# Optimization experiments

Hardware: AMD Instinct MI355X
Metric: run time of the kernel (lower is better)

The kernel has to match this reference:

```python
import jax, jax.numpy as jnp
import numpy as np

N_NODES = 50000
N_EDGES = 1600000
IN_DIM = 1024
MID_DIM = 256


def setup_inputs() -> dict:
    key = jax.random.key(0)
    k1, k2, k3, k4 = jax.random.split(key, 4)
    x = jax.random.normal(k1, (N_NODES, IN_DIM), dtype=jnp.float32)
    edge_index = jax.random.randint(k2, (2, N_EDGES), 0, N_NODES, dtype=jnp.int64)
    # Glorot-style init like PyG GCNConv
    W1 = jax.random.normal(k3, (IN_DIM, MID_DIM), dtype=jnp.float32) * (2.0 / (IN_DIM + MID_DIM)) ** 0.5
    W2 = jax.random.normal(k4, (MID_DIM, IN_DIM), dtype=jnp.float32) * (2.0 / (MID_DIM + IN_DIM)) ** 0.5
    b1 = jnp.zeros((MID_DIM,), dtype=jnp.float32)
    b2 = jnp.zeros((IN_DIM,), dtype=jnp.float32)
    return {"x": x, "edge_index": edge_index, "W1": W1, "b1": b1, "W2": W2, "b2": b2}


def _gcn_conv(x, W, b, src, dst, norm, n):
    # PyG GCNConv: linear transform first, then normalized neighbor sum, then bias.
    xw = x @ W                                   # [N, F_out]
    msg = xw[src] * norm[:, None]                # gather + scale, [E+N, F_out]
    out = jax.ops.segment_sum(msg, dst, num_segments=n)
    return out + b


def reference(x, edge_index, W1, b1, W2, b2):
    n = x.shape[0]
    loops = jnp.arange(n, dtype=edge_index.dtype)
    src = jnp.concatenate([edge_index[0], loops])
    dst = jnp.concatenate([edge_index[1], loops])
    # symmetric normalization with self-loops: D^-1/2 (A+I) D^-1/2
    deg = jax.ops.segment_sum(jnp.ones_like(dst, dtype=x.dtype), dst, num_segments=n)
    dis = jnp.where(deg > 0, jax.lax.rsqrt(jnp.maximum(deg, 1.0)), 0.0)
    norm = dis[src] * dis[dst]                   # [E+N]
    h = jax.nn.relu(_gcn_conv(x, W1, b1, src, dst, norm, n))
    # F.dropout(training=False) is identity at inference
    out = _gcn_conv(h, W2, b2, src, dst, norm, n)
    return out
```

## Files before the change

### kernel.cpp

```cpp
#include <hip/hip_runtime.h>

typedef unsigned short u16;
typedef u16 u16x8 __attribute__((ext_vector_type(8)));
typedef u16 u16x4 __attribute__((ext_vector_type(4)));
typedef short s16x8 __attribute__((ext_vector_type(8)));
typedef float f32x4 __attribute__((ext_vector_type(4)));

__device__ __forceinline__ float b2f(u16 u) {
  unsigned int v = ((unsigned int)u) << 16;
  return __builtin_bit_cast(float, v);
}
__device__ __forceinline__ u16 f2b(float f) {
  unsigned int u = __builtin_bit_cast(unsigned int, f);
  u += 0x7FFFu + ((u >> 16) & 1u);
  return (u16)(u >> 16);
}

__global__ void deg_kernel(const int* __restrict__ dst, int* __restrict__ deg, int E, int n) {
  int e = blockIdx.x * 256 + threadIdx.x;
  if (e < E) {
    int d = dst[e];
    d = min(max(d, 0), n - 1);
    atomicAdd(&deg[d], 1);
  }
}

__global__ void dis_kernel(const int* __restrict__ deg, float* __restrict__ dis, int n) {
  int i = blockIdx.x * 256 + threadIdx.x;
  if (i < n) dis[i] = 1.0f / sqrtf((float)(deg[i] + 1));
}

__global__ __launch_bounds__(256) void scanA(const int* __restrict__ cnt, int* __restrict__ bsum, int n) {
  __shared__ int s[256];
  int t = threadIdx.x, i = blockIdx.x * 256 + t;
  s[t] = (i < n) ? cnt[i] : 0;
  __syncthreads();
  for (int off = 128; off > 0; off >>= 1) {
    if (t < off) s[t] += s[t + off];
    __syncthreads();
  }
  if (t == 0) bsum[blockIdx.x] = s[0];
}

__global__ __launch_bounds__(256) void scanB(int* __restrict__ bsum, int nb) {
  __shared__ int s[256];
  int t = threadIdx.x;
  int v = (t < nb) ? bsum[t] : 0;
  s[t] = v;
  __syncthreads();
  for (int off = 1; off < 256; off <<= 1) {
    int x = (t >= off) ? s[t - off] : 0;
    __syncthreads();
    s[t] += x;
    __syncthreads();
  }
  if (t < nb) bsum[t] = s[t] - v;
}

__global__ __launch_bounds__(256) void scanC(const int* __restrict__ cnt, const int* __restrict__ bsum,
                                             int* __restrict__ rowp, int n) {
  __shared__ int s[256];
  int t = threadIdx.x, i = blockIdx.x * 256 + t;
  int v = (i < n) ? cnt[i] : 0;
  s[t] = v;
  __syncthreads();
  for (int off = 1; off < 256; off <<= 1) {
    int x = (t >= off) ? s[t - off] : 0;
    __syncthreads();
    s[t] += x;
    __syncthreads();
  }
  if (i < n) rowp[i + 1] = bsum[blockIdx.x] + s[t];
  if (i == 0) rowp[0] = 0;
}

__global__ void fill_kernel(const int* __restrict__ src, const int* __restrict__ dst,
                            const int* __restrict__ rowp, int* __restrict__ fill,
                            const float* __restrict__ dis, int* __restrict__ csr_s,
                            float* __restrict__ csr_w, int E, int n) {
  int e = blockIdx.x * 256 + threadIdx.x;
  if (e < E) {
    int s = src[e]; s = min(max(s, 0), n - 1);
    int d = dst[e]; d = min(max(d, 0), n - 1);
    int pos = rowp[d] + atomicAdd(&fill[d], 1);
    csr_s[pos] = s;
    csr_w[pos] = dis[s] * dis[d];
  }
}

__global__ void transpose_cvt(const float* __restrict__ in, u16* __restrict__ out, int K, int N) {
  int idx = blockIdx.x * 256 + threadIdx.x;
  if (idx < K * N) {
    int k = idx / N, nn = idx - k * N;
    out[(size_t)nn * K + k] = f2b(in[idx]);
  }
}

template <bool A_F32, bool OUT_F32>
__global__ __launch_bounds__(256) void gemm_kernel(const void* __restrict__ Ap,
                                                   const u16* __restrict__ BT,
                                                   const float* __restrict__ bias,
                                                   void* __restrict__ Cp, int M, int N, int K) {
  __shared__ u16 As[2][128 * 40];
  __shared__ u16 Bs[2][128 * 40];
  const int tid = threadIdx.x;
  const int m0 = blockIdx.y * 128, n0 = blockIdx.x * 128;
  const int lane = tid & 63, wv = tid >> 6;
  const int wr = (wv >> 1) * 64, wc = (wv & 1) * 64;
  const int q = lane >> 4, l = lane & 15;
  f32x4 acc[4][4] = {};

  float4 aregf[4];
  u16x8 aregb[2];
  u16x8 breg[2];

  auto load_tile = [&](int kt) {
    if (A_F32) {
      const float* A = (const float*)Ap;
#pragma unroll
      for (int i = 0; i < 4; i++) {
        int t = tid + i * 256;
        int r = t >> 3, k4 = (t & 7) * 4;
        int gr = m0 + r;
        aregf[i] = make_float4(0.f, 0.f, 0.f, 0.f);
        if (gr < M) aregf[i] = *(const float4*)&A[(size_t)gr * K + kt + k4];
      }
    } else {
      const u16* A = (const u16*)Ap;
#pragma unroll
      for (int i = 0; i < 2; i++) {
        int t = tid + i * 256;
        int r = t >> 2, k8 = (t & 3) * 8;
        int gr = m0 + r;
        aregb[i] = (u16x8){};
        if (gr < M) aregb[i] = *(const u16x8*)&A[(size_t)gr * K + kt + k8];
      }
    }
#pragma unroll
    for (int i = 0; i < 2; i++) {
      int t = tid + i * 256;
      int r = t >> 2, k8 = (t & 3) * 8;
      breg[i] = *(const u16x8*)&BT[(size_t)(n0 + r) * K + kt + k8];
    }
  };

  auto store_tile = [&](int buf) {
    if (A_F32) {
#pragma unroll
      for (int i = 0; i < 4; i++) {
        int t = tid + i * 256;
        int r = t >> 3, k4 = (t & 7) * 4;
        u16x4 o;
        o[0] = f2b(aregf[i].x); o[1] = f2b(aregf[i].y);
        o[2] = f2b(aregf[i].z); o[3] = f2b(aregf[i].w);
        *(u16x4*)&As[buf][r * 40 + k4] = o;
      }
    } else {
#pragma unroll
      for (int i = 0; i < 2; i++) {
        int t = tid + i * 256;
        int r = t >> 2, k8 = (t & 3) * 8;
        *(u16x8*)&As[buf][r * 40 + k8] = aregb[i];
      }
    }
#pragma unroll
    for (int i = 0; i < 2; i++) {
      int t = tid + i * 256;
      int r = t >> 2, k8 = (t & 3) * 8;
      *(u16x8*)&Bs[buf][r * 40 + k8] = breg[i];
    }
  };

  load_tile(0);
  store_tile(0);
  __syncthreads();

  int cur = 0;
  for (int kt = 0; kt < K; kt += 32) {
    const bool has_next = (kt + 32) < K;
    if (has_next) load_tile(kt + 32);

    s16x8 af[4], bf[4];
#pragma unroll
    for (int mi = 0; mi < 4; mi++) af[mi] = *(const s16x8*)&As[cur][(wr + mi * 16 + l) * 40 + q * 8];
#pragma unroll
    for (int ni = 0; ni < 4; ni++) bf[ni] = *(const s16x8*)&Bs[cur][(wc + ni * 16 + l) * 40 + q * 8];
#pragma unroll
    for (int mi = 0; mi < 4; mi++)
#pragma unroll
      for (int ni = 0; ni < 4; ni++)
        acc[mi][ni] = __builtin_amdgcn_mfma_f32_16x16x32_bf16(af[mi], bf[ni], acc[mi][ni], 0, 0, 0);

    if (has_next) store_tile(cur ^ 1);
    __syncthreads();
    cur ^= 1;
  }

#pragma unroll
  for (int ni = 0; ni < 4; ni++) {
    int col = n0 + wc + ni * 16 + l;
    float bv = bias ? bias[col] : 0.f;
#pragma unroll
    for (int mi = 0; mi < 4; mi++) {
#pragma unroll
      for (int j = 0; j < 4; j++) {
        int row = m0 + wr + mi * 16 + q * 4 + j;
        if (row < M) {
          float v = acc[mi][ni][j] + bv;
          if (OUT_F32)
            ((float*)Cp)[(size_t)row * N + col] = v;
          else
            ((u16*)Cp)[(size_t)row * N + col] = f2b(v);
        }
      }
    }
  }
}

template <bool RELU>
__global__ __launch_bounds__(256) void agg_kernel(const u16* __restrict__ tab,
                                                  const int* __restrict__ rowp,
                                                  const int* __restrict__ csr_s,
                                                  const float* __restrict__ csr_w,
                                                  const float* __restrict__ dis,
                                                  const float* __restrict__ bias,
                                                  u16* __restrict__ out, int n) {
  int wv = threadIdx.x >> 6, lane = threadIdx.x & 63;
  int node = blockIdx.x * 4 + wv;
  if (node >= n) return;
  int f0 = lane * 4;
  float sw = dis[node];
  sw *= sw;
  u16x4 v = *(const u16x4*)&tab[(size_t)node * 256 + f0];
  float a0 = sw * b2f(v[0]), a1 = sw * b2f(v[1]), a2 = sw * b2f(v[2]), a3 = sw * b2f(v[3]);
  int e0 = rowp[node], e1 = rowp[node + 1];
  int e = e0;
  for (; e + 4 <= e1; e += 4) {
    int s0 = csr_s[e], s1 = csr_s[e + 1], s2 = csr_s[e + 2], s3 = csr_s[e + 3];
    float w0 = csr_w[e], w1 = csr_w[e + 1], w2 = csr_w[e + 2], w3 = csr_w[e + 3];
    u16x4 u0 = *(const u16x4*)&tab[(size_t)s0 * 256 + f0];
    u16x4 u1 = *(const u16x4*)&tab[(size_t)s1 * 256 + f0];
    u16x4 u2 = *(const u16x4*)&tab[(size_t)s2 * 256 + f0];
    u16x4 u3 = *(const u16x4*)&tab[(size_t)s3 * 256 + f0];
    a0 += w0 * b2f(u0[0]) + w1 * b2f(u1[0]) + w2 * b2f(u2[0]) + w3 * b2f(u3[0]);
    a1 += w0 * b2f(u0[1]) + w1 * b2f(u1[1]) + w2 * b2f(u2[1]) + w3 * b2f(u3[1]);
    a2 += w0 * b2f(u0[2]) + w1 * b2f(u1[2]) + w2 * b2f(u2[2]) + w3 * b2f(u3[2]);
    a3 += w0 * b2f(u0[3]) + w1 * b2f(u1[3]) + w2 * b2f(u2[3]) + w3 * b2f(u3[3]);
  }
  for (; e < e1; e++) {
    int s = csr_s[e];
    float w = csr_w[e];
    u16x4 u = *(const u16x4*)&tab[(size_t)s * 256 + f0];
    a0 += w * b2f(u[0]);
    a1 += w * b2f(u[1]);
    a2 += w * b2f(u[2]);
    a3 += w * b2f(u[3]);
  }
  if (RELU) {
    a0 = fmaxf(a0 + bias[f0 + 0], 0.f);
    a1 = fmaxf(a1 + bias[f0 + 1], 0.f);
    a2 = fmaxf(a2 + bias[f0 + 2], 0.f);
    a3 = fmaxf(a3 + bias[f0 + 3], 0.f);
  }
  u16x4 o;
  o[0] = f2b(a0); o[1] = f2b(a1); o[2] = f2b(a2); o[3] = f2b(a3);
  *(u16x4*)&out[(size_t)node * 256 + f0] = o;
}

extern "C" void kernel_launch(void* const* d_in, const int* in_sizes, int n_in,
                              void* d_out, int out_size, void* d_ws, size_t ws_size,
                              hipStream_t stream) {
  const float* x  = (const float*)d_in[0];
  const int*   ei = (const int*)d_in[1];
  const float* W1 = (const float*)d_in[2];
  const float* b1 = (const float*)d_in[3];
  const float* W2 = (const float*)d_in[4];
  const float* b2 = (const float*)d_in[5];

  const int MID = in_sizes[3];
  const int IN  = in_sizes[5];
  const int n   = in_sizes[0] / IN;
  const int E   = in_sizes[1] / 2;
  const int* srcv = ei;
  const int* dstv = ei + E;

  char* w = (char*)d_ws;
  size_t off = 0;
  auto alloc = [&](size_t bytes) -> void* {
    void* p = w + off;
    off += (bytes + 255) & ~(size_t)255;
    return p;
  };
  int*   deg   = (int*)alloc((size_t)n * 4);
  int*   rowp  = (int*)alloc((size_t)(n + 1) * 4);
  int*   fill  = (int*)alloc((size_t)n * 4);
  int*   bsum  = (int*)alloc(1024);
  int*   csr_s = (int*)alloc((size_t)E * 4);
  float* csr_w = (float*)alloc((size_t)E * 4);
  float* dis   = (float*)alloc((size_t)n * 4);
  u16*   W1T   = (u16*)alloc((size_t)IN * MID * 2);
  u16*   W2T   = (u16*)alloc((size_t)IN * MID * 2);
  u16*   xw    = (u16*)alloc((size_t)n * MID * 2);
  u16*   h     = (u16*)alloc((size_t)n * MID * 2);
  u16*   ah    = xw;

  hipMemsetAsync(deg, 0, (size_t)n * 4, stream);
  hipMemsetAsync(fill, 0, (size_t)n * 4, stream);

  transpose_cvt<<<(IN * MID + 255) / 256, 256, 0, stream>>>(W1, W1T, IN, MID);
  transpose_cvt<<<(IN * MID + 255) / 256, 256, 0, stream>>>(W2, W2T, MID, IN);

  const int nb = (n + 255) / 256;
  deg_kernel<<<(E + 255) / 256, 256, 0, stream>>>(dstv, deg, E, n);
  dis_kernel<<<nb, 256, 0, stream>>>(deg, dis, n);
  scanA<<<nb, 256, 0, stream>>>(deg, bsum, n);
  scanB<<<1, 256, 0, stream>>>(bsum, nb);
  scanC<<<nb, 256, 0, stream>>>(deg, bsum, rowp, n);
  fill_kernel<<<(E + 255) / 256, 256, 0, stream>>>(srcv, dstv, rowp, fill, dis, csr_s, csr_w, E, n);

  dim3 g1(MID / 128, (n + 127) / 128);
  gemm_kernel<true, false><<<g1, 256, 0, stream>>>(x, W1T, nullptr, xw, n, MID, IN);
  agg_kernel<true><<<(n + 3) / 4, 256, 0, stream>>>(xw, rowp, csr_s, csr_w, dis, b1, h, n);
  agg_kernel<false><<<(n + 3) / 4, 256, 0, stream>>>(h, rowp, csr_s, csr_w, dis, nullptr, ah, n);
  dim3 g2(IN / 128, (n + 127) / 128);
  gemm_kernel<false, true><<<g2, 256, 0, stream>>>(ah, W2T, b2, d_out, n, IN, MID);
}
```

Before: 878.6 us.

## Deepen GEMM prefetch, use hardware bf16 pack conversion, unroll aggregation by eight

The GEMM now keeps two register sets of global tile loads in flight, so loads for tile k+2 are issued while tile k is computed. It also replaces the explicit barrier with an lgkmcnt wait plus a raw s_barrier. The fp32-to-bf16 conversion uses the v_cvt_pk_bf16_f32 instruction instead of the software rounding routine. The aggregation kernel gathers eight neighbor rows per iteration instead of four to expose more memory-level parallelism. The trade-off is higher register pressure, which may lower occupancy, and the inline asm conversion may round differently at edge cases.

```diff
diff --git a/kernel.cpp b/kernel.cpp
--- a/kernel.cpp
+++ b/kernel.cpp
@@ -110,11 +110,11 @@
   const int q = lane >> 4, l = lane & 15;
   f32x4 acc[4][4] = {};
 
-  float4 aregf[4];
-  u16x8 aregb[2];
-  u16x8 breg[2];
-
-  auto load_tile = [&](int kt) {
+  float4 af0[4], af1[4];
+  u16x8 ab0[2], ab1[2];
+  u16x8 br0[2], br1[2];
+
+  auto load_tile = [&](float4 (&af)[4], u16x8 (&ab)[2], u16x8 (&br)[2], int kt) {
     if (A_F32) {
       const float* A = (const float*)Ap;
 #pragma unroll
@@ -122,8 +122,8 @@
         int t = tid + i * 256;
         int r = t >> 3, k4 = (t & 7) * 4;
         int gr = m0 + r;
-        aregf[i] = make_float4(0.f, 0.f, 0.f, 0.f);
-        if (gr < M) aregf[i] = *(const float4*)&A[(size_t)gr * K + kt + k4];
+        af[i] = make_float4(0.f, 0.f, 0.f, 0.f);
+        if (gr < M) af[i] = *(const float4*)&A[(size_t)gr * K + kt + k4];
       }
     } else {
       const u16* A = (const u16*)Ap;
@@ -132,68 +132,81 @@
         int t = tid + i * 256;
         int r = t >> 2, k8 = (t & 3) * 8;
         int gr = m0 + r;
-        aregb[i] = (u16x8){};
-        if (gr < M) aregb[i] = *(const u16x8*)&A[(size_t)gr * K + kt + k8];
+        ab[i] = (u16x8){};
+        if (gr < M) ab[i] = *(const u16x8*)&A[(size_t)gr * K + kt + k8];
       }
     }
 #pragma unroll
     for (int i = 0; i < 2; i++) {
       int t = tid + i * 256;
       int r = t >> 2, k8 = (t & 3) * 8;
-      breg[i] = *(const u16x8*)&BT[(size_t)(n0 + r) * K + kt + k8];
-    }
-  };
-
-  auto store_tile = [&](int buf) {
+      br[i] = *(const u16x8*)&BT[(size_t)(n0 + r) * K + kt + k8];
+    }
+  };
+
+  auto store_tile = [&](float4 (&af)[4], u16x8 (&ab)[2], u16x8 (&br)[2], int buf) {
     if (A_F32) {
 #pragma unroll
       for (int i = 0; i < 4; i++) {
         int t = tid + i * 256;
         int r = t >> 3, k4 = (t & 7) * 4;
-        u16x4 o;
-        o[0] = f2b(aregf[i].x); o[1] = f2b(aregf[i].y);
-        o[2] = f2b(aregf[i].z); o[3] = f2b(aregf[i].w);
-        *(u16x4*)&As[buf][r * 40 + k4] = o;
+        unsigned int lo, hi;
+        asm("v_cvt_pk_bf16_f32 %0, %1, %2" : "=v"(lo) : "v"(af[i].x), "v"(af[i].y));
+        asm("v_cvt_pk_bf16_f32 %0, %1, %2" : "=v"(hi) : "v"(af[i].z), "v"(af[i].w));
+        uint2 o; o.x = lo; o.y = hi;
+        *(uint2*)&As[buf][r * 40 + k4] = o;
       }
     } else {
 #pragma unroll
       for (int i = 0; i < 2; i++) {
         int t = tid + i * 256;
         int r = t >> 2, k8 = (t & 3) * 8;
-        *(u16x8*)&As[buf][r * 40 + k8] = aregb[i];
+        *(u16x8*)&As[buf][r * 40 + k8] = ab[i];
       }
     }
 #pragma unroll
     for (int i = 0; i < 2; i++) {
       int t = tid + i * 256;
       int r = t >> 2, k8 = (t & 3) * 8;
-      *(u16x8*)&Bs[buf][r * 40 + k8] = breg[i];
-    }
-  };
-
-  load_tile(0);
-  store_tile(0);
-  __syncthreads();
-
-  int cur = 0;
-  for (int kt = 0; kt < K; kt += 32) {
-    const bool has_next = (kt + 32) < K;
-    if (has_next) load_tile(kt + 32);
-
-    s16x8 af[4], bf[4];
-#pragma unroll
-    for (int mi = 0; mi < 4; mi++) af[mi] = *(const s16x8*)&As[cur][(wr + mi * 16 + l) * 40 + q * 8];
-#pragma unroll
-    for (int ni = 0; ni < 4; ni++) bf[ni] = *(const s16x8*)&Bs[cur][(wc + ni * 16 + l) * 40 + q * 8];
+      *(u16x8*)&Bs[buf][r * 40 + k8] = br[i];
+    }
+  };
+
+  auto compute = [&](int buf) {
+    s16x8 afr[4], bfr[4];
+#pragma unroll
+    for (int mi = 0; mi < 4; mi++) afr[mi] = *(const s16x8*)&As[buf][(wr + mi * 16 + l) * 40 + q * 8];
+#pragma unroll
+    for (int ni = 0; ni < 4; ni++) bfr[ni] = *(const s16x8*)&Bs[buf][(wc + ni * 16 + l) * 40 + q * 8];
 #pragma unroll
     for (int mi = 0; mi < 4; mi++)
 #pragma unroll
       for (int ni = 0; ni < 4; ni++)
-        acc[mi][ni] = __builtin_amdgcn_mfma_f32_16x16x32_bf16(af[mi], bf[ni], acc[mi][ni], 0, 0, 0);
-
-    if (has_next) store_tile(cur ^ 1);
-    __syncthreads();
-    cur ^= 1;
+        acc[mi][ni] = __builtin_amdgcn_mfma_f32_16x16x32_bf16(afr[mi], bfr[ni], acc[mi][ni], 0, 0, 0);
+  };
+
+  auto bar = [&]() {
+    asm volatile("s_waitcnt lgkmcnt(0)" ::: "memory");
+    __builtin_amdgcn_s_barrier();
+  };
+
+  const int nt = K >> 5;
+  load_tile(af0, ab0, br0, 0);
+  if (nt > 1) load_tile(af1, ab1, br1, 32);
+  store_tile(af0, ab0, br0, 0);
+  bar();
+
+  for (int t = 0; t < nt; t += 2) {
+    if (t + 2 < nt) load_tile(af0, ab0, br0, (t + 2) << 5);
+    compute(0);
+    if (t + 1 < nt) store_tile(af1, ab1, br1, 1);
+    bar();
+    if (t + 1 < nt) {
+      if (t + 3 < nt) load_tile(af1, ab1, br1, (t + 3) << 5);
+      compute(1);
+      if (t + 2 < nt) store_tile(af0, ab0, br0, 0);
+      bar();
+    }
   }
 
 #pragma unroll
@@ -235,17 +248,21 @@
   float a0 = sw * b2f(v[0]), a1 = sw * b2f(v[1]), a2 = sw * b2f(v[2]), a3 = sw * b2f(v[3]);
   int e0 = rowp[node], e1 = rowp[node + 1];
   int e = e0;
-  for (; e + 4 <= e1; e += 4) {
-    int s0 = csr_s[e], s1 = csr_s[e + 1], s2 = csr_s[e + 2], s3 = csr_s[e + 3];
-    float w0 = csr_w[e], w1 = csr_w[e + 1], w2 = csr_w[e + 2], w3 = csr_w[e + 3];
-    u16x4 u0 = *(const u16x4*)&tab[(size_t)s0 * 256 + f0];
-    u16x4 u1 = *(const u16x4*)&tab[(size_t)s1 * 256 + f0];
-    u16x4 u2 = *(const u16x4*)&tab[(size_t)s2 * 256 + f0];
-    u16x4 u3 = *(const u16x4*)&tab[(size_t)s3 * 256 + f0];
-    a0 += w0 * b2f(u0[0]) + w1 * b2f(u1[0]) + w2 * b2f(u2[0]) + w3 * b2f(u3[0]);
-    a1 += w0 * b2f(u0[1]) + w1 * b2f(u1[1]) + w2 * b2f(u2[1]) + w3 * b2f(u3[1]);
-    a2 += w0 * b2f(u0[2]) + w1 * b2f(u1[2]) + w2 * b2f(u2[2]) + w3 * b2f(u3[2]);
-    a3 += w0 * b2f(u0[3]) + w1 * b2f(u1[3]) + w2 * b2f(u2[3]) + w3 * b2f(u3[3]);
+  for (; e + 8 <= e1; e += 8) {
+    int s[8];
+    float wt[8];
+    u16x4 u[8];
+#pragma unroll
+    for (int j = 0; j < 8; j++) { s[j] = csr_s[e + j]; wt[j] = csr_w[e + j]; }
+#pragma unroll
+    for (int j = 0; j < 8; j++) u[j] = *(const u16x4*)&tab[(size_t)s[j] * 256 + f0];
+#pragma unroll
+    for (int j = 0; j < 8; j++) {
+      a0 += wt[j] * b2f(u[j][0]);
+      a1 += wt[j] * b2f(u[j][1]);
+      a2 += wt[j] * b2f(u[j][2]);
+      a3 += wt[j] * b2f(u[j][3]);
+    }
   }
   for (; e < e1; e++) {
     int s = csr_s[e];
```

Measured after the change: 924.4 us. 1.05x slower.
